# Performance work log

Hardware: AMD Instinct MI355X
Metric: run time of the kernel (lower is better)

The kernel has to match this reference:

```python
import jax, jax.numpy as jnp
import numpy as np

LEAK = 0.1

def _l2n(x):
    return x / (jnp.linalg.norm(x) + 1e-12)

def _sn_weight(W, u):
    # torch spectral_norm: one power iteration from buffer u, u/v detached,
    # grad flows through W via sigma = u' W v.
    v = jax.lax.stop_gradient(_l2n(W.T @ u))
    u2 = jax.lax.stop_gradient(_l2n(W @ v))
    sigma = u2 @ (W @ v)
    return W / sigma

def _conv1x1(x, W, b):
    # x: (B,C,H,W), W: (O,C) -> (B,O,H,W)
    return jnp.einsum('oc,bchw->bohw', W, x) + b[None, :, None, None]

def _sn_layer(x, W, b, u):
    return jax.nn.leaky_relu(_conv1x1(x, _sn_weight(W, u), b), LEAK)

def _attention(x, qW, qb, kW, kb, vW, vb, gamma):
    B, C, H, Wd = x.shape
    N = H * Wd
    q = _conv1x1(x, qW, qb).reshape(B, -1, N)   # (B, C//8, N)
    k = _conv1x1(x, kW, kb).reshape(B, -1, N)   # (B, C//8, N)
    v = _conv1x1(x, vW, vb).reshape(B, C, N)    # (B, C, N)
    # energy[b,n,m] = sum_c q[b,c,n] * k[b,c,m]  (query^T key)
    energy = jnp.einsum('bcn,bcm->bnm', q, k)
    amap = jax.nn.softmax(energy, axis=-1)
    # aw[b,c,m] = sum_n v[b,c,n] * amap[b,m,n]   (bmm(v, amap^T))
    aw = jnp.einsum('bcn,bmn->bcm', v, amap).reshape(B, C, H, Wd)
    return gamma * aw + x


def setup_inputs() -> dict:
    key = jax.random.key(0)
    ks = iter(jax.random.split(key, 64))
    def nrm(shape, s=0.05):
        return jax.random.normal(next(ks), shape, jnp.float32) * s
    d = {'input': jax.random.normal(next(ks), (4, 6, 64, 64), jnp.float32)}
    dims = [(6, 64), (64, 128), (128, 256), (256, 512), (512, 1)]
    for i, (cin, cout) in enumerate(dims, 1):
        d[f'W{i}'] = nrm((cout, cin))
        d[f'b{i}'] = nrm((cout,))
        d[f'u{i}'] = _l2n(jax.random.normal(next(ks), (cout,), jnp.float32))
    for tag, C in (('a1', 256), ('a2', 512)):
        d[f'{tag}_qW'] = nrm((C // 8, C)); d[f'{tag}_qb'] = nrm((C // 8,))
        d[f'{tag}_kW'] = nrm((C // 8, C)); d[f'{tag}_kb'] = nrm((C // 8,))
        d[f'{tag}_vW'] = nrm((C, C));      d[f'{tag}_vb'] = nrm((C,))
        d[f'{tag}_gamma'] = jnp.full((1,), 0.1, jnp.float32)
    return d


def reference(input, W1, b1, u1, W2, b2, u2, W3, b3, u3, W4, b4, u4, W5, b5, u5,
              a1_qW, a1_qb, a1_kW, a1_kb, a1_vW, a1_vb, a1_gamma,
              a2_qW, a2_qb, a2_kW, a2_kb, a2_vW, a2_vb, a2_gamma):
    out = _sn_layer(input, W1, b1, u1)
    out = _sn_layer(out, W2, b2, u2)
    out = _sn_layer(out, W3, b3, u3)
    out = _attention(out, a1_qW, a1_qb, a1_kW, a1_kb, a1_vW, a1_vb, a1_gamma)
    out = _sn_layer(out, W4, b4, u4)
    out = _attention(out, a2_qW, a2_qb, a2_kW, a2_kb, a2_vW, a2_vb, a2_gamma)
    out = _sn_layer(out, W5, b5, u5)
    return out.squeeze()  # (B, H, W)
```

## Files before the change

### kernel.cpp

```cpp
#include <hip/hip_runtime.h>
#include <math.h>

#define N_PIX 4096
#define BATCH 4
#define LOG2E 1.4426950408889634f

typedef __bf16 bf16x8 __attribute__((ext_vector_type(8)));
typedef __bf16 bf16x4v __attribute__((ext_vector_type(4)));
typedef float f32x4 __attribute__((ext_vector_type(4)));

__device__ __forceinline__ unsigned pack4_fp8(float a, float b, float c, float d) {
    unsigned p = __builtin_amdgcn_cvt_pk_fp8_f32(a, b, 0, false);
    p = __builtin_amdgcn_cvt_pk_fp8_f32(c, d, p, true);
    return p;
}
__device__ __forceinline__ uint8_t to_fp8(float v) {
    return (uint8_t)(__builtin_amdgcn_cvt_pk_fp8_f32(v, v, 0, false) & 0xff);
}

struct SigP {
    const float* W[5];
    const float* u[5];
    int O[5];
    int C[5];
};

__device__ __forceinline__ void sig_map(int bid, int& L, int& ch) {
    if (bid == 0)      { L = 0; ch = 0; }
    else if (bid < 3)  { L = 1; ch = bid - 1; }
    else if (bid < 7)  { L = 2; ch = bid - 3; }
    else if (bid < 15) { L = 3; ch = bid - 7; }
    else               { L = 4; ch = 0; }
}

__global__ __launch_bounds__(256)
void sigma_p1(SigP p, float* __restrict__ ybuf) {
    __shared__ float ush[64];
    int L, ch;
    sig_map(blockIdx.x, L, ch);
    const float* W = p.W[L];
    const float* u = p.u[L];
    int O = p.O[L], C = p.C[L];
    int o0 = ch * 64;
    int no = O - o0; if (no > 64) no = 64;
    int t = threadIdx.x;
    if (t < 64) ush[t] = (t < no) ? u[o0 + t] : 0.f;
    __syncthreads();
    for (int c = t; c < C; c += 256) {
        float a = 0.f;
        for (int o = 0; o < no; ++o) a += W[(size_t)(o0 + o) * C + c] * ush[o];
        atomicAdd(&ybuf[L * 512 + c], a);
    }
}

__global__ __launch_bounds__(256)
void sigma_p2(SigP p, const float* __restrict__ ybuf,
              float* __restrict__ S1, float* __restrict__ S2) {
    __shared__ float ysh[512];
    int L, ch;
    sig_map(blockIdx.x, L, ch);
    const float* W = p.W[L];
    int O = p.O[L], C = p.C[L];
    int o0 = ch * 64;
    int o_hi = o0 + 64; if (o_hi > O) o_hi = O;
    int t = threadIdx.x;
    int lane = t & 63, w = t >> 6;
    for (int c = t; c < C; c += 256) ysh[c] = ybuf[L * 512 + c];
    __syncthreads();

    if (ch == 0) {
        float s = 0.f;
        for (int c = t; c < C; c += 256) s += ysh[c] * ysh[c];
        #pragma unroll
        for (int off = 1; off < 64; off <<= 1) s += __shfl_xor(s, off);
        if (lane == 0) atomicAdd(&S1[L], s);
    }

    float sq = 0.f;
    for (int i = 0; i < 16; ++i) {
        int o = o0 + w * 16 + i;
        if (o >= o_hi) break;
        float a = 0.f;
        for (int c = lane; c < C; c += 64) a += W[(size_t)o * C + c] * ysh[c];
        #pragma unroll
        for (int off = 1; off < 64; off <<= 1) a += __shfl_xor(a, off);
        if (lane == 0) sq += a * a;
    }
    if (lane == 0) atomicAdd(&S2[L], sq);
}

__global__ __launch_bounds__(256)
void wsplit_kernel(const float* __restrict__ W, const float* __restrict__ iv,
                   float scale, int C, __bf16* __restrict__ out) {
    int o = blockIdx.x;
    float s = (iv ? iv[0] : 1.f) * scale;
    for (int c = threadIdx.x; c < C; c += 256) {
        float wv = W[(size_t)o * C + c] * s;
        __bf16 hi = (__bf16)wv;
        float lo = wv - (float)hi;
        out[(size_t)o * 2 * C + c] = hi;
        out[(size_t)o * 2 * C + C + c] = (__bf16)lo;
    }
}

__global__ __launch_bounds__(256)
void concat_bias(const float* __restrict__ qb1, const float* __restrict__ kb1,
                 const float* __restrict__ qb2, const float* __restrict__ kb2,
                 float* __restrict__ bb,
                 const float* __restrict__ S1, const float* __restrict__ S2,
                 float* __restrict__ sig) {
    int t = threadIdx.x;
    if (t < 32) bb[t] = qb1[t] * LOG2E;
    else if (t < 64) bb[t] = kb1[t - 32];
    else if (t < 128) bb[t] = qb2[t - 64] * LOG2E;
    else if (t < 192) bb[t] = kb2[t - 128];
    else if (t >= 224 && t < 229) {
        int L = t - 224;
        float rinv = 1.f / (sqrtf(S1[L]) + 1e-12f);
        float ns2 = rinv * rinv * S2[L];
        float sg = ns2 / (sqrtf(ns2) + 1e-12f);
        sig[L] = 1.f / sg;
    }
}

__global__ __launch_bounds__(256)
void conv_f32_kernel(const float* __restrict__ x, const float* __restrict__ W,
                     const float* __restrict__ bias, const float* __restrict__ sig,
                     float* __restrict__ out, int C, int O, int lrelu) {
    __shared__ float Ws[16][68];
    __shared__ float Xs[16][68];
    int t = threadIdx.x;
    int tx = t & 15, ty = t >> 4;
    int b = blockIdx.z;
    int n0 = blockIdx.x * 64, o0 = blockIdx.y * 64;
    float acc[4][4] = {};
    const float* xb = x + (size_t)b * C * N_PIX;
    for (int c0 = 0; c0 < C; c0 += 16) {
        #pragma unroll
        for (int i = 0; i < 4; ++i) {
            int e = t + i * 256;
            int o = e >> 4, c = e & 15;
            float wv = 0.f;
            if (o0 + o < O && c0 + c < C) wv = W[(size_t)(o0 + o) * C + c0 + c];
            Ws[c][o] = wv;
        }
        #pragma unroll
        for (int i = 0; i < 4; ++i) {
            int e = t + i * 256;
            int c = e >> 6, n = e & 63;
            float xv = 0.f;
            if (c0 + c < C) xv = xb[(size_t)(c0 + c) * N_PIX + n0 + n];
            Xs[c][n] = xv;
        }
        __syncthreads();
        #pragma unroll
        for (int cc = 0; cc < 16; ++cc) {
            float4 wv = *(const float4*)&Ws[cc][ty * 4];
            float4 xv = *(const float4*)&Xs[cc][tx * 4];
            float wa[4] = {wv.x, wv.y, wv.z, wv.w};
            float xa[4] = {xv.x, xv.y, xv.z, xv.w};
            #pragma unroll
            for (int i = 0; i < 4; ++i)
                #pragma unroll
                for (int j = 0; j < 4; ++j)
                    acc[i][j] += wa[i] * xa[j];
        }
        __syncthreads();
    }
    float ivv = sig ? sig[0] : 1.f;
    for (int i = 0; i < 4; ++i) {
        int o = o0 + ty * 4 + i;
        if (o >= O) break;
        float bv = bias[o];
        float vres[4];
        #pragma unroll
        for (int j = 0; j < 4; ++j) {
            float v = acc[i][j] * ivv + bv;
            if (lrelu) v = (v > 0.f) ? v : 0.1f * v;
            vres[j] = v;
        }
        *(float4*)&out[((size_t)b * O + o) * N_PIX + n0 + tx * 4] =
            make_float4(vres[0], vres[1], vres[2], vres[3]);
    }
}

__global__ __launch_bounds__(256)
void tsplit64_kernel(const float* __restrict__ in, __bf16* __restrict__ out) {
    __shared__ float tile[64 * 65];
    int t = threadIdx.x;
    int n0 = blockIdx.x * 64, b = blockIdx.y;
    for (int e = t; e < 64 * 64; e += 256) {
        int c = e >> 6, n = e & 63;
        tile[n * 65 + c] = in[((size_t)b * 64 + c) * N_PIX + n0 + n];
    }
    __syncthreads();
    for (int e = t; e < 64 * 64; e += 256) {
        int n = e >> 6, c = e & 63;
        float v = tile[n * 65 + c];
        __bf16 hi = (__bf16)v;
        size_t base = ((size_t)b * N_PIX + n0 + n) * 128;
        out[base + c] = hi;
        out[base + 64 + c] = (__bf16)(v - (float)hi);
    }
}

template <int WO, int WN, int MF, int MODE, int IN_F32, int LRELU>
__global__ __launch_bounds__(256)
void mfma_conv(const void* __restrict__ xt, const __bf16* __restrict__ wsp,
               const float* __restrict__ bias, float bscale,
               void* __restrict__ outp, int C, int O) {
    constexpr int NT_BLK = WN * 128;
    constexpr int OT_BLK = WO * 16 * MF;
    __shared__ __bf16 Ws[OT_BLK * 72];
    __shared__ __bf16 Xs[NT_BLK * 72];
    int t = threadIdx.x;
    int lane = t & 63, w = t >> 6;
    int l15 = lane & 15, quad = lane >> 4;
    int wo = w / WN, wn = w % WN;
    int b = blockIdx.z;
    int n0b = blockIdx.x * NT_BLK, o0b = blockIdx.y * OT_BLK;

    f32x4 acc[MF][8] = {};

    for (int c0 = 0; c0 < C; c0 += 32) {
        __syncthreads();
        for (int e = t; e < OT_BLK * 8; e += 256) {
            int row = e >> 3, part = e & 7;
            size_t src = (size_t)(o0b + row) * 2 * C +
                         (part < 4 ? c0 + part * 8 : C + c0 + (part - 4) * 8);
            int dst = row * 72 + (part < 4 ? part * 8 : 32 + (part - 4) * 8);
            *(uint4*)&Ws[dst] = *(const uint4*)&wsp[src];
        }
        if (IN_F32) {
            const float* xf = (const float*)xt;
            for (int e = t; e < NT_BLK * 8; e += 256) {
                int row = e >> 3, part = e & 7;
                float4 v = *(const float4*)&xf[((size_t)b * N_PIX + n0b + row) * C + c0 + part * 4];
                bf16x4v hi, lo;
                float va[4] = {v.x, v.y, v.z, v.w};
                #pragma unroll
                for (int j = 0; j < 4; ++j) {
                    hi[j] = (__bf16)va[j];
                    lo[j] = (__bf16)(va[j] - (float)hi[j]);
                }
                *(bf16x4v*)&Xs[row * 72 + part * 4] = hi;
                *(bf16x4v*)&Xs[row * 72 + 32 + part * 4] = lo;
            }
        } else {
            const __bf16* xb = (const __bf16*)xt;
            for (int e = t; e < NT_BLK * 8; e += 256) {
                int row = e >> 3, part = e & 7;
                size_t src = ((size_t)b * N_PIX + n0b + row) * 2 * C +
                             (part < 4 ? c0 + part * 8 : C + c0 + (part - 4) * 8);
                int dst = row * 72 + (part < 4 ? part * 8 : 32 + (part - 4) * 8);
                *(uint4*)&Xs[dst] = *(const uint4*)&xb[src];
            }
        }
        __syncthreads();

        bf16x8 ah[MF], al[MF];
        #pragma unroll
        for (int mf = 0; mf < MF; ++mf) {
            int base = (wo * 16 * MF + mf * 16 + l15) * 72 + quad * 8;
            ah[mf] = *(const bf16x8*)&Ws[base];
            al[mf] = *(const bf16x8*)&Ws[base + 32];
        }
        #pragma unroll
        for (int nt = 0; nt < 8; ++nt) {
            int bbase = (wn * 128 + nt * 16 + l15) * 72 + quad * 8;
            bf16x8 bh = *(const bf16x8*)&Xs[bbase];
            bf16x8 bl = *(const bf16x8*)&Xs[bbase + 32];
            #pragma unroll
            for (int mf = 0; mf < MF; ++mf) {
                acc[mf][nt] = __builtin_amdgcn_mfma_f32_16x16x32_bf16(ah[mf], bh, acc[mf][nt], 0, 0, 0);
                acc[mf][nt] = __builtin_amdgcn_mfma_f32_16x16x32_bf16(ah[mf], bl, acc[mf][nt], 0, 0, 0);
                acc[mf][nt] = __builtin_amdgcn_mfma_f32_16x16x32_bf16(al[mf], bh, acc[mf][nt], 0, 0, 0);
            }
        }
    }

    float bv[MF][4];
    #pragma unroll
    for (int mf = 0; mf < MF; ++mf)
        #pragma unroll
        for (int r = 0; r < 4; ++r)
            bv[mf][r] = bias[o0b + wo * 16 * MF + mf * 16 + quad * 4 + r] * bscale;

    #pragma unroll
    for (int mf = 0; mf < MF; ++mf)
        #pragma unroll
        for (int nt = 0; nt < 8; ++nt) {
            int n = n0b + wn * 128 + nt * 16 + l15;
            float val[4];
            #pragma unroll
            for (int r = 0; r < 4; ++r) {
                float v = acc[mf][nt][r] + bv[mf][r];
                if (LRELU) v = (v > 0.f) ? v : 0.1f * v;
                val[r] = v;
            }
            int obase = o0b + wo * 16 * MF + mf * 16 + quad * 4;
            if (MODE == 1) {
                uint8_t* ob = (uint8_t*)outp;
                #pragma unroll
                for (int r = 0; r < 4; ++r)
                    ob[((size_t)b * O + obase + r) * N_PIX + n] = to_fp8(val[r]);
            } else if (MODE == 2) {
                __bf16* ob = (__bf16*)outp;
                bf16x4v hv, lv;
                #pragma unroll
                for (int r = 0; r < 4; ++r) {
                    hv[r] = (__bf16)val[r];
                    lv[r] = (__bf16)(val[r] - (float)hv[r]);
                }
                size_t rb = ((size_t)b * N_PIX + n) * 2 * O + obase;
                *(bf16x4v*)&ob[rb] = hv;
                *(bf16x4v*)&ob[rb + O] = lv;
            } else {
                __bf16* ob = (__bf16*)outp;
                bf16x4v hv;
                #pragma unroll
                for (int r = 0; r < 4; ++r) hv[r] = (__bf16)val[r];
                *(bf16x4v*)&ob[((size_t)b * N_PIX + n) * O + obase] = hv;
            }
        }
}

template <int CQ>
__global__ __launch_bounds__(256)
void s_gemm(const __bf16* __restrict__ qt, const __bf16* __restrict__ kt,
            uint8_t* __restrict__ S, int QSTR) {
    constexpr int NKK = CQ / 32;
    __shared__ uint8_t Ss[128 * 144];
    int t = threadIdx.x;
    int lane = t & 63, w = t >> 6;
    int l15 = lane & 15, quad = lane >> 4;
    int k0 = blockIdx.x * 128, q0 = blockIdx.y * 128, b = blockIdx.z;

    bf16x8 kf[2][NKK], qf[8][NKK];
    #pragma unroll
    for (int mf = 0; mf < 2; ++mf)
        #pragma unroll
        for (int kk = 0; kk < NKK; ++kk)
            kf[mf][kk] = *(const bf16x8*)&kt[((size_t)b * N_PIX + k0 + w * 32 + mf * 16 + l15) * QSTR + kk * 32 + quad * 8];
    #pragma unroll
    for (int nt = 0; nt < 8; ++nt)
        #pragma unroll
        for (int kk = 0; kk < NKK; ++kk)
            qf[nt][kk] = *(const bf16x8*)&qt[((size_t)b * N_PIX + q0 + nt * 16 + l15) * QSTR + kk * 32 + quad * 8];

    f32x4 acc[2][8] = {};
    #pragma unroll
    for (int kk = 0; kk < NKK; ++kk)
        #pragma unroll
        for (int mf = 0; mf < 2; ++mf)
            #pragma unroll
            for (int nt = 0; nt < 8; ++nt)
                acc[mf][nt] = __builtin_amdgcn_mfma_f32_16x16x32_bf16(kf[mf][kk], qf[nt][kk], acc[mf][nt], 0, 0, 0);

    #pragma unroll
    for (int mf = 0; mf < 2; ++mf)
        #pragma unroll
        for (int nt = 0; nt < 8; ++nt) {
            unsigned p = pack4_fp8(exp2f(acc[mf][nt][0]), exp2f(acc[mf][nt][1]),
                                   exp2f(acc[mf][nt][2]), exp2f(acc[mf][nt][3]));
            *(unsigned*)&Ss[(nt * 16 + l15) * 144 + w * 32 + mf * 16 + quad * 4] = p;
        }
    __syncthreads();
    int ql = t >> 1, kh = (t & 1) * 64;
    size_t row = ((size_t)b * N_PIX + q0 + ql) * (size_t)N_PIX + k0 + kh;
    #pragma unroll
    for (int j = 0; j < 4; ++j)
        *(uint4*)&S[row + j * 16] = *(const uint4*)&Ss[ql * 144 + kh + j * 16];
}

typedef __attribute__((address_space(1))) const void* gas1_t;
typedef __attribute__((address_space(3))) void* las3_t;

template <int NT>
__global__ __launch_bounds__(1024)
void pv_gemm12(const uint8_t* __restrict__ E, const uint8_t* __restrict__ vg,
               const __bf16* __restrict__ xin2,
               const float* __restrict__ gamma, float* __restrict__ out, int C) {
    constexpr int CCH = NT * 32;
    __shared__ uint8_t PshA[256 * 128];
    __shared__ uint8_t PshB[256 * 128];
    __shared__ uint8_t VshA[CCH * 128];
    __shared__ uint8_t VshB[CCH * 128];
    int t = threadIdx.x;
    int lane = t & 63, w = t >> 6;
    int l15 = lane & 15, quad = lane >> 4;
    int qs = w & 7, cs = w >> 3;
    int bid = blockIdx.x;
    int pair = bid & 63, cblk = bid >> 6;
    int qi = pair >> 2, b = pair & 3;
    int q0 = qi * 256, c0 = cblk * CCH;
    const uint8_t* Pb = E + ((size_t)b * N_PIX + q0) * (size_t)N_PIX;
    const uint8_t* Vb = vg + ((size_t)b * C + c0) * (size_t)N_PIX;

    int r8 = lane >> 3;
    int cgl = (lane & 7) ^ r8;

    const long ONES = 0x3838383838383838L;

    f32x4 acc[2][NT] = {};
    f32x4 acc_s[2] = {};

    auto stage = [&](uint8_t* Ps, uint8_t* Vs, int k0) {
        #pragma unroll
        for (int ch = 0; ch < 2; ++ch) {
            int row0 = w * 16 + ch * 8;
            const uint8_t* g = Pb + (size_t)(row0 + r8) * N_PIX + k0 + cgl * 16;
            __builtin_amdgcn_global_load_lds((gas1_t)g, (las3_t)&Ps[row0 * 128], 16, 0, 0);
        }
        if (w < CCH / 8) {
            int row0 = w * 8;
            const uint8_t* g = Vb + (size_t)(row0 + r8) * N_PIX + k0 + cgl * 16;
            __builtin_amdgcn_global_load_lds((gas1_t)g, (las3_t)&Vs[row0 * 128], 16, 0, 0);
        }
    };

    auto compute = [&](const uint8_t* Ps, const uint8_t* Vs) {
        #pragma unroll
        for (int kk = 0; kk < 4; ++kk) {
            long pa[2];
            #pragma unroll
            for (int mf = 0; mf < 2; ++mf) {
                int row = qs * 32 + mf * 16 + l15;
                int cg = (2 * kk + (quad >> 1)) ^ (row & 7);
                pa[mf] = *(const long*)&Ps[row * 128 + cg * 16 + (quad & 1) * 8];
            }
            #pragma unroll
            for (int mf = 0; mf < 2; ++mf)
                acc_s[mf] = __builtin_amdgcn_mfma_f32_16x16x32_fp8_fp8(pa[mf], ONES, acc_s[mf], 0, 0, 0);
            #pragma unroll
            for (int nt = 0; nt < NT; ++nt) {
                int row = cs * (NT * 16) + nt * 16 + l15;
                int cg = (2 * kk + (quad >> 1)) ^ (row & 7);
                long vf = *(const long*)&Vs[row * 128 + cg * 16 + (quad & 1) * 8];
                #pragma unroll
                for (int mf = 0; mf < 2; ++mf)
                    acc[mf][nt] = __builtin_amdgcn_mfma_f32_16x16x32_fp8_fp8(pa[mf], vf, acc[mf][nt], 0, 0, 0);
            }
        }
    };

    stage(PshA, VshA, 0);
    __syncthreads();

    for (int k0 = 0; k0 < N_PIX; k0 += 256) {
        stage(PshB, VshB, k0 + 128);
        compute(PshA, VshA);
        __syncthreads();
        if (k0 + 256 < N_PIX) stage(PshA, VshA, k0 + 256);
        compute(PshB, VshB);
        __syncthreads();
    }

    float g = gamma[0];
    #pragma unroll
    for (int mf = 0; mf < 2; ++mf)
        #pragma unroll
        for (int r = 0; r < 4; ++r) {
            int ql = qs * 32 + mf * 16 + quad * 4 + r;
            int q = q0 + ql;
            float gil = g / acc_s[mf][r];
            size_t xrb = ((size_t)b * N_PIX + q) * 2 * C;
            size_t orb = ((size_t)b * N_PIX + q) * C;
            #pragma unroll
            for (int nt = 0; nt < NT; ++nt) {
                int c = c0 + cs * (NT * 16) + nt * 16 + l15;
                float xr = (float)xin2[xrb + c] + (float)xin2[xrb + C + c];
                out[orb + c] = gil * acc[mf][nt][r] + xr;
            }
        }
}

__global__ __launch_bounds__(256)
void l5_kernel(const float* __restrict__ h, const float* __restrict__ W5,
               const float* __restrict__ b5, const float* __restrict__ sig,
               float* __restrict__ out) {
    int t = threadIdx.x;
    int lane = t & 63, w = t >> 6;
    int p = blockIdx.x * 4 + w;
    const float* row = h + (size_t)p * 512;
    float4 a0 = *(const float4*)&row[lane * 8];
    float4 a1 = *(const float4*)&row[lane * 8 + 4];
    float4 w0 = *(const float4*)&W5[lane * 8];
    float4 w1 = *(const float4*)&W5[lane * 8 + 4];
    float s = a0.x * w0.x + a0.y * w0.y + a0.z * w0.z + a0.w * w0.w +
              a1.x * w1.x + a1.y * w1.y + a1.z * w1.z + a1.w * w1.w;
    #pragma unroll
    for (int off = 1; off < 64; off <<= 1) s += __shfl_xor(s, off);
    if (lane == 0) {
        float v = sig[0] * s + b5[0];
        out[p] = (v > 0.f) ? v : 0.1f * v;
    }
}

extern "C" void kernel_launch(void* const* d_in, const int* in_sizes, int n_in,
                              void* d_out, int out_size, void* d_ws, size_t ws_size,
                              hipStream_t stream) {
    const float* x   = (const float*)d_in[0];
    const float* W1  = (const float*)d_in[1];
    const float* b1  = (const float*)d_in[2];
    const float* u1  = (const float*)d_in[3];
    const float* W2  = (const float*)d_in[4];
    const float* b2  = (const float*)d_in[5];
    const float* u2  = (const float*)d_in[6];
    const float* W3  = (const float*)d_in[7];
    const float* b3  = (const float*)d_in[8];
    const float* u3  = (const float*)d_in[9];
    const float* W4  = (const float*)d_in[10];
    const float* b4  = (const float*)d_in[11];
    const float* u4  = (const float*)d_in[12];
    const float* W5  = (const float*)d_in[13];
    const float* b5  = (const float*)d_in[14];
    const float* u5  = (const float*)d_in[15];
    const float* a1_qW = (const float*)d_in[16];
    const float* a1_qb = (const float*)d_in[17];
    const float* a1_kW = (const float*)d_in[18];
    const float* a1_kb = (const float*)d_in[19];
    const float* a1_vW = (const float*)d_in[20];
    const float* a1_vb = (const float*)d_in[21];
    const float* a1_g  = (const float*)d_in[22];
    const float* a2_qW = (const float*)d_in[23];
    const float* a2_qb = (const float*)d_in[24];
    const float* a2_kW = (const float*)d_in[25];
    const float* a2_kb = (const float*)d_in[26];
    const float* a2_vW = (const float*)d_in[27];
    const float* a2_vb = (const float*)d_in[28];
    const float* a2_g  = (const float*)d_in[29];

    float* ws = (float*)d_ws;
    const size_t NF = (size_t)BATCH * N_PIX;
    float* sig    = ws;
    float* h1     = ws + 16;
    float* slabC  = h1 + NF * 64;
    float* slabS1 = slabC + NF * 512;
    float* slabS2 = slabS1 + NF * 256;
    float* qtf    = slabS2 + NF * 512;
    float* ktf    = qtf + NF * 32;
    float* wspf   = ktf + NF * 32;
    float* bbf    = wspf + 592000;
    float* ysig   = wspf + 592256;
    float* Sf     = wspf + 600000;

    __bf16* h1t = (__bf16*)slabS1;
    __bf16* h2t = (__bf16*)slabS2;
    __bf16* h3t = (__bf16*)slabS1;
    __bf16* h5t = (__bf16*)slabS2;
    float*  h4t = slabC;
    uint8_t* vb1 = (uint8_t*)(slabC + NF * 256);
    float*  h6t = slabC;
    uint8_t* vb2 = (uint8_t*)slabS1;
    __bf16* qkt = (__bf16*)qtf;
    __bf16* wsp = (__bf16*)wspf;
    uint8_t* Sbuf = (uint8_t*)Sf;

    float* ybuf = ysig;
    float* S1v  = ysig + 2560;
    float* S2v  = ysig + 2576;

    __bf16* wsL2  = wsp;
    __bf16* wsL3  = wsL2 + 16384;
    __bf16* wsL4  = wsL3 + 65536;
    __bf16* wsA1q = wsL4 + 262144;
    __bf16* wsA1k = wsA1q + 16384;
    __bf16* wsA1v = wsA1k + 16384;
    __bf16* wsA2q = wsA1v + 131072;
    __bf16* wsA2k = wsA2q + 65536;
    __bf16* wsA2v = wsA2k + 65536;

    dim3 blk(256);

    SigP sp;
    sp.W[0] = W1; sp.u[0] = u1; sp.O[0] = 64;  sp.C[0] = 6;
    sp.W[1] = W2; sp.u[1] = u2; sp.O[1] = 128; sp.C[1] = 64;
    sp.W[2] = W3; sp.u[2] = u3; sp.O[2] = 256; sp.C[2] = 128;
    sp.W[3] = W4; sp.u[3] = u4; sp.O[3] = 512; sp.C[3] = 256;
    sp.W[4] = W5; sp.u[4] = u5; sp.O[4] = 1;   sp.C[4] = 512;

    hipMemsetAsync(ysig, 0, 2592 * sizeof(float), stream);
    sigma_p1<<<dim3(16), blk, 0, stream>>>(sp, ybuf);
    sigma_p2<<<dim3(16), blk, 0, stream>>>(sp, ybuf, S1v, S2v);
    concat_bias<<<1, blk, 0, stream>>>(a1_qb, a1_kb, a2_qb, a2_kb, bbf, S1v, S2v, sig);

    wsplit_kernel<<<128, blk, 0, stream>>>(W2, sig + 1, 1.f, 64, wsL2);
    wsplit_kernel<<<256, blk, 0, stream>>>(W3, sig + 2, 1.f, 128, wsL3);
    wsplit_kernel<<<512, blk, 0, stream>>>(W4, sig + 3, 1.f, 256, wsL4);
    wsplit_kernel<<<32,  blk, 0, stream>>>(a1_qW, nullptr, LOG2E, 256, wsA1q);
    wsplit_kernel<<<32,  blk, 0, stream>>>(a1_kW, nullptr, 1.f, 256, wsA1k);
    wsplit_kernel<<<256, blk, 0, stream>>>(a1_vW, nullptr, 1.f, 256, wsA1v);
    wsplit_kernel<<<64,  blk, 0, stream>>>(a2_qW, nullptr, LOG2E, 512, wsA2q);
    wsplit_kernel<<<64,  blk, 0, stream>>>(a2_kW, nullptr, 1.f, 512, wsA2k);
    wsplit_kernel<<<512, blk, 0, stream>>>(a2_vW, nullptr, 1.f, 512, wsA2v);

    conv_f32_kernel<<<dim3(64, 1, 4), blk, 0, stream>>>(x, W1, b1, sig + 0, h1, 6, 64, 1);
    tsplit64_kernel<<<dim3(64, 4), blk, 0, stream>>>(h1, h1t);

    mfma_conv<4, 1, 1, 2, 0, 1><<<dim3(32, 2, 4), blk, 0, stream>>>(h1t, wsL2, b2, 1.f, h2t, 64, 128);
    mfma_conv<4, 1, 1, 2, 0, 1><<<dim3(32, 4, 4), blk, 0, stream>>>(h2t, wsL3, b3, 1.f, h3t, 128, 256);

    mfma_conv<2, 2, 1, 4, 0, 0><<<dim3(16, 2, 4), blk, 0, stream>>>(h3t, wsA1q, bbf, 1.f, qkt, 256, 64);
    mfma_conv<4, 1, 1, 1, 0, 0><<<dim3(32, 4, 4), blk, 0, stream>>>(h3t, wsA1v, a1_vb, 1.f, vb1, 256, 256);
    s_gemm<32><<<dim3(32, 32, 4), blk, 0, stream>>>(qkt, qkt + 32, Sbuf, 64);
    pv_gemm12<2><<<dim3(256), dim3(1024), 0, stream>>>(Sbuf, vb1, h3t, a1_g, h4t, 256);

    mfma_conv<4, 1, 1, 2, 1, 1><<<dim3(32, 8, 4), blk, 0, stream>>>(h4t, wsL4, b4, 1.f, h5t, 256, 512);

    mfma_conv<2, 2, 1, 4, 0, 0><<<dim3(16, 4, 4), blk, 0, stream>>>(h5t, wsA2q, bbf + 64, 1.f, qkt, 512, 128);
    mfma_conv<4, 1, 1, 1, 0, 0><<<dim3(32, 8, 4), blk, 0, stream>>>(h5t, wsA2v, a2_vb, 1.f, vb2, 512, 512);
    s_gemm<64><<<dim3(32, 32, 4), blk, 0, stream>>>(qkt, qkt + 64, Sbuf, 128);
    pv_gemm12<4><<<dim3(256), dim3(1024), 0, stream>>>(Sbuf, vb2, h5t, a2_g, h6t, 512);

    l5_kernel<<<4096, blk, 0, stream>>>(h6t, W5, b5, sig + 4, (float*)d_out);
}
```

Before: 551.5 us.

## Loop s_gemm over key tiles and parameterize pv_gemm query-row tiling

s_gemm now keeps its query fragments in registers and loops over four 128-wide key tiles per block. This cuts block count and repeated Q loads, and it computes each output column group with a small accumulator to reduce register pressure. pv_gemm is generalized to a QROWS parameter. The first attention layer now uses 128 query rows with wider channel chunks, which changes the P/V reuse balance and the grid split. The trade-offs are extra barriers per key tile and fewer blocks in s_gemm.

```diff
diff --git a/kernel.cpp b/kernel.cpp
--- a/kernel.cpp
+++ b/kernel.cpp
@@ -325,75 +325,82 @@
         }
 }
 
-template <int CQ>
-__global__ __launch_bounds__(256)
-void s_gemm(const __bf16* __restrict__ qt, const __bf16* __restrict__ kt,
-            uint8_t* __restrict__ S, int QSTR) {
+template <int CQ, int KITER>
+__global__ __launch_bounds__(256)
+void s_gemm2(const __bf16* __restrict__ qt, const __bf16* __restrict__ kt,
+             uint8_t* __restrict__ S, int QSTR) {
     constexpr int NKK = CQ / 32;
     __shared__ uint8_t Ss[128 * 144];
     int t = threadIdx.x;
     int lane = t & 63, w = t >> 6;
     int l15 = lane & 15, quad = lane >> 4;
-    int k0 = blockIdx.x * 128, q0 = blockIdx.y * 128, b = blockIdx.z;
-
-    bf16x8 kf[2][NKK], qf[8][NKK];
-    #pragma unroll
-    for (int mf = 0; mf < 2; ++mf)
-        #pragma unroll
-        for (int kk = 0; kk < NKK; ++kk)
-            kf[mf][kk] = *(const bf16x8*)&kt[((size_t)b * N_PIX + k0 + w * 32 + mf * 16 + l15) * QSTR + kk * 32 + quad * 8];
+    int kbase = blockIdx.x * KITER * 128, q0 = blockIdx.y * 128, b = blockIdx.z;
+
+    bf16x8 qf[8][NKK];
     #pragma unroll
     for (int nt = 0; nt < 8; ++nt)
         #pragma unroll
         for (int kk = 0; kk < NKK; ++kk)
             qf[nt][kk] = *(const bf16x8*)&qt[((size_t)b * N_PIX + q0 + nt * 16 + l15) * QSTR + kk * 32 + quad * 8];
 
-    f32x4 acc[2][8] = {};
-    #pragma unroll
-    for (int kk = 0; kk < NKK; ++kk)
+    for (int ki = 0; ki < KITER; ++ki) {
+        int k0 = kbase + ki * 128;
+        bf16x8 kf[2][NKK];
         #pragma unroll
         for (int mf = 0; mf < 2; ++mf)
             #pragma unroll
-            for (int nt = 0; nt < 8; ++nt)
-                acc[mf][nt] = __builtin_amdgcn_mfma_f32_16x16x32_bf16(kf[mf][kk], qf[nt][kk], acc[mf][nt], 0, 0, 0);
-
-    #pragma unroll
-    for (int mf = 0; mf < 2; ++mf)
+            for (int kk = 0; kk < NKK; ++kk)
+                kf[mf][kk] = *(const bf16x8*)&kt[((size_t)b * N_PIX + k0 + w * 32 + mf * 16 + l15) * QSTR + kk * 32 + quad * 8];
+
         #pragma unroll
         for (int nt = 0; nt < 8; ++nt) {
-            unsigned p = pack4_fp8(exp2f(acc[mf][nt][0]), exp2f(acc[mf][nt][1]),
-                                   exp2f(acc[mf][nt][2]), exp2f(acc[mf][nt][3]));
-            *(unsigned*)&Ss[(nt * 16 + l15) * 144 + w * 32 + mf * 16 + quad * 4] = p;
-        }
-    __syncthreads();
-    int ql = t >> 1, kh = (t & 1) * 64;
-    size_t row = ((size_t)b * N_PIX + q0 + ql) * (size_t)N_PIX + k0 + kh;
-    #pragma unroll
-    for (int j = 0; j < 4; ++j)
-        *(uint4*)&S[row + j * 16] = *(const uint4*)&Ss[ql * 144 + kh + j * 16];
+            f32x4 a[2] = {};
+            #pragma unroll
+            for (int kk = 0; kk < NKK; ++kk)
+                #pragma unroll
+                for (int mf = 0; mf < 2; ++mf)
+                    a[mf] = __builtin_amdgcn_mfma_f32_16x16x32_bf16(kf[mf][kk], qf[nt][kk], a[mf], 0, 0, 0);
+            #pragma unroll
+            for (int mf = 0; mf < 2; ++mf) {
+                unsigned p = pack4_fp8(exp2f(a[mf][0]), exp2f(a[mf][1]),
+                                       exp2f(a[mf][2]), exp2f(a[mf][3]));
+                *(unsigned*)&Ss[(nt * 16 + l15) * 144 + w * 32 + mf * 16 + quad * 4] = p;
+            }
+        }
+        __syncthreads();
+        int ql = t >> 1, kh = (t & 1) * 64;
+        size_t row = ((size_t)b * N_PIX + q0 + ql) * (size_t)N_PIX + k0 + kh;
+        #pragma unroll
+        for (int j = 0; j < 4; ++j)
+            *(uint4*)&S[row + j * 16] = *(const uint4*)&Ss[ql * 144 + kh + j * 16];
+        __syncthreads();
+    }
 }
 
 typedef __attribute__((address_space(1))) const void* gas1_t;
 typedef __attribute__((address_space(3))) void* las3_t;
 
-template <int NT>
+template <int NT, int QROWS>
 __global__ __launch_bounds__(1024)
-void pv_gemm12(const uint8_t* __restrict__ E, const uint8_t* __restrict__ vg,
+void pv_gemm13(const uint8_t* __restrict__ E, const uint8_t* __restrict__ vg,
                const __bf16* __restrict__ xin2,
                const float* __restrict__ gamma, float* __restrict__ out, int C) {
-    constexpr int CCH = NT * 32;
-    __shared__ uint8_t PshA[256 * 128];
-    __shared__ uint8_t PshB[256 * 128];
+    constexpr int NQS = QROWS / 32;
+    constexpr int NCS = 16 / NQS;
+    constexpr int CCH = NT * 16 * NCS;
+    constexpr int NPAIR = (N_PIX / QROWS) * BATCH;
+    __shared__ uint8_t PshA[QROWS * 128];
+    __shared__ uint8_t PshB[QROWS * 128];
     __shared__ uint8_t VshA[CCH * 128];
     __shared__ uint8_t VshB[CCH * 128];
     int t = threadIdx.x;
     int lane = t & 63, w = t >> 6;
     int l15 = lane & 15, quad = lane >> 4;
-    int qs = w & 7, cs = w >> 3;
+    int qs = w % NQS, cs = w / NQS;
     int bid = blockIdx.x;
-    int pair = bid & 63, cblk = bid >> 6;
+    int pair = bid % NPAIR, cblk = bid / NPAIR;
     int qi = pair >> 2, b = pair & 3;
-    int q0 = qi * 256, c0 = cblk * CCH;
+    int q0 = qi * QROWS, c0 = cblk * CCH;
     const uint8_t* Pb = E + ((size_t)b * N_PIX + q0) * (size_t)N_PIX;
     const uint8_t* Vb = vg + ((size_t)b * C + c0) * (size_t)N_PIX;
 
@@ -407,12 +414,13 @@
 
     auto stage = [&](uint8_t* Ps, uint8_t* Vs, int k0) {
         #pragma unroll
-        for (int ch = 0; ch < 2; ++ch) {
-            int row0 = w * 16 + ch * 8;
+        for (int ch = 0; ch < QROWS / 128; ++ch) {
+            int row0 = w * (QROWS / 16) + ch * 8;
             const uint8_t* g = Pb + (size_t)(row0 + r8) * N_PIX + k0 + cgl * 16;
             __builtin_amdgcn_global_load_lds((gas1_t)g, (las3_t)&Ps[row0 * 128], 16, 0, 0);
         }
-        if (w < CCH / 8) {
+        static_assert(CCH / 8 == 16, "V staging assumes 16 chunks");
+        {
             int row0 = w * 8;
             const uint8_t* g = Vb + (size_t)(row0 + r8) * N_PIX + k0 + cgl * 16;
             __builtin_amdgcn_global_load_lds((gas1_t)g, (las3_t)&Vs[row0 * 128], 16, 0, 0);
@@ -603,15 +611,15 @@
 
     mfma_conv<2, 2, 1, 4, 0, 0><<<dim3(16, 2, 4), blk, 0, stream>>>(h3t, wsA1q, bbf, 1.f, qkt, 256, 64);
     mfma_conv<4, 1, 1, 1, 0, 0><<<dim3(32, 4, 4), blk, 0, stream>>>(h3t, wsA1v, a1_vb, 1.f, vb1, 256, 256);
-    s_gemm<32><<<dim3(32, 32, 4), blk, 0, stream>>>(qkt, qkt + 32, Sbuf, 64);
-    pv_gemm12<2><<<dim3(256), dim3(1024), 0, stream>>>(Sbuf, vb1, h3t, a1_g, h4t, 256);
+    s_gemm2<32, 4><<<dim3(8, 32, 4), blk, 0, stream>>>(qkt, qkt + 32, Sbuf, 64);
+    pv_gemm13<2, 128><<<dim3(256), dim3(1024), 0, stream>>>(Sbuf, vb1, h3t, a1_g, h4t, 256);
 
     mfma_conv<4, 1, 1, 2, 1, 1><<<dim3(32, 8, 4), blk, 0, stream>>>(h4t, wsL4, b4, 1.f, h5t, 256, 512);
 
     mfma_conv<2, 2, 1, 4, 0, 0><<<dim3(16, 4, 4), blk, 0, stream>>>(h5t, wsA2q, bbf + 64, 1.f, qkt, 512, 128);
     mfma_conv<4, 1, 1, 1, 0, 0><<<dim3(32, 8, 4), blk, 0, stream>>>(h5t, wsA2v, a2_vb, 1.f, vb2, 512, 512);
-    s_gemm<64><<<dim3(32, 32, 4), blk, 0, stream>>>(qkt, qkt + 64, Sbuf, 128);
-    pv_gemm12<4><<<dim3(256), dim3(1024), 0, stream>>>(Sbuf, vb2, h5t, a2_g, h6t, 512);
+    s_gemm2<64, 4><<<dim3(8, 32, 4), blk, 0, stream>>>(qkt, qkt + 64, Sbuf, 128);
+    pv_gemm13<4, 256><<<dim3(256), dim3(1024), 0, stream>>>(Sbuf, vb2, h5t, a2_g, h6t, 512);
 
     l5_kernel<<<4096, blk, 0, stream>>>(h6t, W5, b5, sig + 4, (float*)d_out);
 }
```

After: 528.7 us. 4.1% less time.
